# Kernel optimization log

Measured on AMD Instinct MI355X. Metric: run time of the kernel, lower is better.

Reference implementation:

```python
import jax, jax.numpy as jnp
import numpy as np

N = 100000   # active voxels
K = 27       # 3x3x3 kernel offsets
C = 64       # in_channels == out_channels (residual block)
EPS = 1e-5


def setup_inputs() -> dict:
    key = jax.random.key(0)
    ks = jax.random.split(key, 10)
    feats = jax.random.normal(ks[0], (N, C), dtype=jnp.float32)
    # kernel-map: for each voxel, index of the neighbor voxel for each of the 27 offsets
    nbr = jax.random.randint(ks[1], (N, K), 0, N)
    nbr = nbr.at[:, K // 2].set(jnp.arange(N))  # center offset is identity
    w_scale = 1.0 / np.sqrt(K * C)
    W1 = jax.random.normal(ks[2], (K, C, C), dtype=jnp.float32) * w_scale
    b1 = jax.random.normal(ks[3], (C,), dtype=jnp.float32) * 0.01
    g1 = jnp.ones((C,), jnp.float32)
    be1 = jnp.zeros((C,), jnp.float32)
    W2 = jax.random.normal(ks[4], (K, C, C), dtype=jnp.float32) * w_scale
    b2 = jax.random.normal(ks[5], (C,), dtype=jnp.float32) * 0.01
    g2 = jnp.ones((C,), jnp.float32)
    be2 = jnp.zeros((C,), jnp.float32)
    return {"feats": feats, "nbr": nbr, "W1": W1, "b1": b1, "g1": g1, "be1": be1,
            "W2": W2, "b2": b2, "g2": g2, "be2": be2}


def _sparse_conv(f, nbr, W, b):
    # gather neighbor features per kernel offset: [N, K, C]
    g = f[nbr]
    # per-offset matmul and reduce over offsets (gather-matmul-scatter form)
    return jnp.einsum('nkc,kcd->nd', g, W) + b


def _bn(x, gamma, beta):
    # BatchNorm over active voxels (training-mode batch stats, per channel)
    mu = x.mean(axis=0)
    var = x.var(axis=0)
    return (x - mu) * jax.lax.rsqrt(var + EPS) * gamma + beta


def reference(feats, nbr, W1, b1, g1, be1, W2, b2, g2, be2):
    h = jax.nn.relu(_bn(_sparse_conv(feats, nbr, W1, b1), g1, be1))
    h = _bn(_sparse_conv(h, nbr, W2, b2), g2, be2)
    return jax.nn.relu(h + feats)  # residual add + ReLU
```

## Files before the change

kernel.cpp:

```cpp
#include <hip/hip_runtime.h>

#define NCH 64
#define KOFF 27
#define EPSV 1e-5f

typedef __attribute__((ext_vector_type(8))) short  bf16x8;
typedef __attribute__((ext_vector_type(4))) float  f32x4;
typedef __attribute__((ext_vector_type(8))) unsigned short u16x8;

__device__ __forceinline__ unsigned short f2bf(float x) {
    unsigned int u = __float_as_uint(x);
    u += 0x7fffu + ((u >> 16) & 1u);
    return (unsigned short)(u >> 16);
}

__global__ __launch_bounds__(256)
void prep_kernel(const float* __restrict__ feats,
                 const float* __restrict__ W1, const float* __restrict__ W2,
                 unsigned short* __restrict__ fbf,
                 unsigned short* __restrict__ wt1, unsigned short* __restrict__ wt2,
                 float* __restrict__ stat, int total8)
{
    const int b = blockIdx.x;
    if (b == 0) {
        stat[threadIdx.x] = 0.f;
        return;
    }
    if (b <= 108) {
        const float* W = (b <= 54) ? W1 : W2;
        unsigned short* Wt = (b <= 54) ? wt1 : wt2;
        const int t = (b <= 54 ? b - 1 : b - 55) * 256 + threadIdx.x;
        const int l  = t & 63;
        const int ct = (t >> 6) & 3;
        const int s  = (t >> 8) & 1;
        const int k  = t >> 9;
        const int d     = ct * 16 + (l & 15);
        const int cbase = s * 32 + (l >> 4) * 8;
        u16x8 o;
#pragma unroll
        for (int j = 0; j < 8; ++j)
            o[j] = f2bf(W[(size_t)k * 4096 + (size_t)(cbase + j) * 64 + d]);
        reinterpret_cast<u16x8*>(Wt)[t] = o;
        return;
    }
    const int idx = (b - 109) * 256 + threadIdx.x;
    if (idx >= total8) return;
    const float4* xp = reinterpret_cast<const float4*>(feats) + (size_t)idx * 2;
    const float4 a = xp[0], c = xp[1];
    u16x8 o;
    o[0] = f2bf(a.x); o[1] = f2bf(a.y); o[2] = f2bf(a.z); o[3] = f2bf(a.w);
    o[4] = f2bf(c.x); o[5] = f2bf(c.y); o[6] = f2bf(c.z); o[7] = f2bf(c.w);
    reinterpret_cast<u16x8*>(fbf)[idx] = o;
}

__global__ __launch_bounds__(64, 3)
void conv_mfma_kernel(const unsigned short* __restrict__ fin,
                      const int* __restrict__ nbr,
                      const unsigned short* __restrict__ Wt,
                      const float* __restrict__ bias,
                      float* __restrict__ out, float* __restrict__ pstat, int N)
{
    __shared__ int s_idx[32 * KOFF];

    const int lane = threadIdx.x;
    const int n0   = blockIdx.x * 32;
    const int m    = lane & 15;
    const int quad = lane >> 4;

    {
        const int rem  = N - n0;
        const int maxi = (rem < 32 ? rem : 32) * KOFF;
        const int* nb  = nbr + (size_t)n0 * KOFF;
        for (int p = lane; p < 32 * KOFF; p += 64)
            s_idx[p] = ((p < maxi) ? nb[p] : 0) * (NCH * 2);
    }

    f32x4 acc[2][4];
#pragma unroll
    for (int mt = 0; mt < 2; ++mt)
#pragma unroll
        for (int ct = 0; ct < 4; ++ct) acc[mt][ct] = (f32x4){0.f, 0.f, 0.f, 0.f};

    bf16x8 A[2][2][2];
    bf16x8 B[2][2][4];
    const char* finB = (const char*)fin;

#define LOADK(kk, p)                                                         \
    {                                                                        \
        _Pragma("unroll")                                                    \
        for (int mt = 0; mt < 2; ++mt) {                                     \
            const int ofs = s_idx[(mt * 16 + m) * KOFF + (kk)];              \
            const char* fp = finB + ofs + quad * 16;                         \
            A[p][mt][0] = *reinterpret_cast<const bf16x8*>(fp);              \
            A[p][mt][1] = *reinterpret_cast<const bf16x8*>(fp + 64);         \
        }                                                                    \
        const unsigned short* wp = Wt + (size_t)(kk) * 4096 + lane * 8;      \
        _Pragma("unroll")                                                    \
        for (int s = 0; s < 2; ++s)                                          \
            _Pragma("unroll")                                                \
            for (int ct = 0; ct < 4; ++ct)                                   \
                B[p][s][ct] =                                                \
                    *reinterpret_cast<const bf16x8*>(wp + (s * 4 + ct) * 512);\
    }

#define DOMFMA(p)                                                            \
    {                                                                        \
        _Pragma("unroll")                                                    \
        for (int mt = 0; mt < 2; ++mt)                                       \
            _Pragma("unroll")                                                \
            for (int s = 0; s < 2; ++s)                                      \
                _Pragma("unroll")                                            \
                for (int ct = 0; ct < 4; ++ct)                               \
                    acc[mt][ct] = __builtin_amdgcn_mfma_f32_16x16x32_bf16(   \
                        A[p][mt][s], B[p][s][ct], acc[mt][ct], 0, 0, 0);     \
    }

    LOADK(0, 0);
#pragma unroll 1
    for (int k = 0; k + 2 < KOFF; k += 2) {
        LOADK(k + 1, 1);
        DOMFMA(0);
        LOADK(k + 2, 0);
        DOMFMA(1);
    }
    DOMFMA(0);

#pragma unroll
    for (int ct = 0; ct < 4; ++ct) {
        const int ch = ct * 16 + m;
        const float bv = bias[ch];
        float s = 0.f, q = 0.f;
#pragma unroll
        for (int mt = 0; mt < 2; ++mt) {
#pragma unroll
            for (int r = 0; r < 4; ++r) {
                const int vox = n0 + mt * 16 + quad * 4 + r;
                if (vox < N) {
                    const float v = acc[mt][ct][r] + bv;
                    out[(size_t)vox * NCH + ch] = v;
                    s += v;
                    q += v * v;
                }
            }
        }
        s += __shfl_xor(s, 16, 64);
        s += __shfl_xor(s, 32, 64);
        q += __shfl_xor(q, 16, 64);
        q += __shfl_xor(q, 32, 64);
        if (quad == 0) {
            float* pr = pstat + (size_t)blockIdx.x * 128;
            pr[ch]      = s;
            pr[64 + ch] = q;
        }
    }
#undef LOADK
#undef DOMFMA
}

__global__ __launch_bounds__(256)
void reduce_stats_kernel(const float* __restrict__ pstat, float* __restrict__ stat,
                         int rows)
{
    __shared__ float s_[256];
    const int ch = threadIdx.x & 127;
    const int h  = threadIdx.x >> 7;
    float acc = 0.f;
    for (int r = blockIdx.x * 2 + h; r < rows; r += gridDim.x * 2)
        acc += pstat[(size_t)r * 128 + ch];
    s_[threadIdx.x] = acc;
    __syncthreads();
    if (threadIdx.x < 128)
        atomicAdd(&stat[threadIdx.x], s_[threadIdx.x] + s_[threadIdx.x + 128]);
}

__global__ __launch_bounds__(256)
void bn_relu_bf16_kernel(const float* __restrict__ x, const float* __restrict__ sums,
                         const float* __restrict__ gmm, const float* __restrict__ bet,
                         float invN, unsigned short* __restrict__ y, int total8)
{
    const int idx = blockIdx.x * 256 + threadIdx.x;
    if (idx >= total8) return;
    const int c0 = (idx & 7) * 8;
    const float4* xp = reinterpret_cast<const float4*>(x) + (size_t)idx * 2;
    const float4 a = xp[0], b = xp[1];
    float v[8] = {a.x, a.y, a.z, a.w, b.x, b.y, b.z, b.w};
    u16x8 o;
#pragma unroll
    for (int i = 0; i < 8; ++i) {
        const int c = c0 + i;
        const float mu  = sums[c] * invN;
        const float var = sums[64 + c] * invN - mu * mu;
        const float rs  = rsqrtf(var + EPSV);
        const float sc  = gmm[c] * rs;
        const float sh  = bet[c] - mu * sc;
        o[i] = f2bf(fmaxf(fmaf(v[i], sc, sh), 0.f));
    }
    reinterpret_cast<u16x8*>(y)[idx] = o;
}

__global__ __launch_bounds__(256)
void bn_res_relu_kernel(float* __restrict__ x, const float* __restrict__ feats,
                        const float* __restrict__ sums, const float* __restrict__ gmm,
                        const float* __restrict__ bet, float invN, int total4)
{
    const int idx = blockIdx.x * blockDim.x + threadIdx.x;
    if (idx >= total4) return;
    float4 v = reinterpret_cast<float4*>(x)[idx];
    const float4 f = reinterpret_cast<const float4*>(feats)[idx];
    const int c0 = (idx & 15) * 4;
    float sc[4], sh[4];
#pragma unroll
    for (int i = 0; i < 4; ++i) {
        const int c = c0 + i;
        const float mu  = sums[c] * invN;
        const float var = sums[64 + c] * invN - mu * mu;
        const float rs  = rsqrtf(var + EPSV);
        sc[i] = gmm[c] * rs;
        sh[i] = bet[c] - mu * sc[i];
    }
    v.x = fmaxf(fmaf(v.x, sc[0], sh[0]) + f.x, 0.f);
    v.y = fmaxf(fmaf(v.y, sc[1], sh[1]) + f.y, 0.f);
    v.z = fmaxf(fmaf(v.z, sc[2], sh[2]) + f.z, 0.f);
    v.w = fmaxf(fmaf(v.w, sc[3], sh[3]) + f.w, 0.f);
    reinterpret_cast<float4*>(x)[idx] = v;
}

extern "C" void kernel_launch(void* const* d_in, const int* in_sizes, int n_in,
                              void* d_out, int out_size, void* d_ws, size_t ws_size,
                              hipStream_t stream)
{
    const float* feats = (const float*)d_in[0];
    const int*   nbr   = (const int*)d_in[1];
    const float* W1    = (const float*)d_in[2];
    const float* b1    = (const float*)d_in[3];
    const float* g1    = (const float*)d_in[4];
    const float* be1   = (const float*)d_in[5];
    const float* W2    = (const float*)d_in[6];
    const float* b2    = (const float*)d_in[7];
    const float* g2    = (const float*)d_in[8];
    const float* be2   = (const float*)d_in[9];
    float* out = (float*)d_out;

    const int N  = in_sizes[0] / NCH;
    const int NC = N * NCH;
    const float invN = 1.0f / (float)N;

    float*          h0   = (float*)d_ws;
    unsigned short* fbf  = (unsigned short*)(h0 + NC);
    unsigned short* hbf  = fbf + NC;
    unsigned short* wt1  = hbf + NC;
    unsigned short* wt2  = wt1 + KOFF * 4096;
    float*          stat = (float*)(wt2 + KOFF * 4096);

    const int total8   = NC / 8;
    const int castGrid = (total8 + 255) / 256;
    const int prepGrid = 1 + 108 + castGrid;
    const int convGrid = (N + 31) / 32;

    float* pstat1 = out;
    float* pstat2 = h0;

    prep_kernel<<<prepGrid, 256, 0, stream>>>(feats, W1, W2, fbf, wt1, wt2,
                                              stat, total8);
    conv_mfma_kernel<<<convGrid, 64, 0, stream>>>(fbf, nbr, wt1, b1, h0,
                                                  pstat1, N);
    reduce_stats_kernel<<<32, 256, 0, stream>>>(pstat1, stat, convGrid);
    bn_relu_bf16_kernel<<<castGrid, 256, 0, stream>>>(h0, stat, g1, be1, invN,
                                                      hbf, total8);
    conv_mfma_kernel<<<convGrid, 64, 0, stream>>>(hbf, nbr, wt2, b2, out,
                                                  pstat2, N);
    reduce_stats_kernel<<<32, 256, 0, stream>>>(pstat2, stat + 128, convGrid);
    bn_res_relu_kernel<<<(NC / 4 + 255) / 256, 256, 0, stream>>>(
        out, feats, stat + 128, g2, be2, invN, NC / 4);
}
```

Measured before the change: 296.0 us.

## Deepen gather prefetch pipeline with separate A and B ring buffers

Splits each kernel offset into two K-halves and software-pipelines the loop fully unrolled over 54 steps. Gathered neighbor loads (A) are prefetched 6 steps ahead in a 7-slot ring and weight loads (B) 2 steps ahead in a 3-slot ring. The aim is to hide the latency of the random gathers better than the previous double buffer. The deeper ring and full unroll raise register pressure and code size, which could lower occupancy.

Result: faster. 287.3 us (-3.0%).

```diff
diff --git a/kernel.cpp b/kernel.cpp
--- a/kernel.cpp
+++ b/kernel.cpp
@@ -81,49 +81,48 @@
 #pragma unroll
         for (int ct = 0; ct < 4; ++ct) acc[mt][ct] = (f32x4){0.f, 0.f, 0.f, 0.f};
 
-    bf16x8 A[2][2][2];
-    bf16x8 B[2][2][4];
+    bf16x8 A[7][2];
+    bf16x8 B[3][4];
     const char* finB = (const char*)fin;
 
-#define LOADK(kk, p)                                                         \
+#define LOADA(t, buf)                                                        \
     {                                                                        \
+        const int k_ = (t) >> 1, s_ = (t) & 1;                               \
         _Pragma("unroll")                                                    \
         for (int mt = 0; mt < 2; ++mt) {                                     \
-            const int ofs = s_idx[(mt * 16 + m) * KOFF + (kk)];              \
-            const char* fp = finB + ofs + quad * 16;                         \
-            A[p][mt][0] = *reinterpret_cast<const bf16x8*>(fp);              \
-            A[p][mt][1] = *reinterpret_cast<const bf16x8*>(fp + 64);         \
+            const int ofs = s_idx[(mt * 16 + m) * KOFF + k_];                \
+            A[buf][mt] = *reinterpret_cast<const bf16x8*>(                   \
+                finB + ofs + s_ * 64 + quad * 16);                           \
         }                                                                    \
-        const unsigned short* wp = Wt + (size_t)(kk) * 4096 + lane * 8;      \
+    }
+
+#define LOADB(t, buf)                                                        \
+    {                                                                        \
+        const unsigned short* wp = Wt + (size_t)(t) * 2048 + lane * 8;       \
         _Pragma("unroll")                                                    \
-        for (int s = 0; s < 2; ++s)                                          \
-            _Pragma("unroll")                                                \
-            for (int ct = 0; ct < 4; ++ct)                                   \
-                B[p][s][ct] =                                                \
-                    *reinterpret_cast<const bf16x8*>(wp + (s * 4 + ct) * 512);\
-    }
-
-#define DOMFMA(p)                                                            \
+        for (int ct = 0; ct < 4; ++ct)                                       \
+            B[buf][ct] = *reinterpret_cast<const bf16x8*>(wp + ct * 512);    \
+    }
+
+#define DOMFMA(t)                                                            \
     {                                                                        \
         _Pragma("unroll")                                                    \
         for (int mt = 0; mt < 2; ++mt)                                       \
             _Pragma("unroll")                                                \
-            for (int s = 0; s < 2; ++s)                                      \
-                _Pragma("unroll")                                            \
-                for (int ct = 0; ct < 4; ++ct)                               \
-                    acc[mt][ct] = __builtin_amdgcn_mfma_f32_16x16x32_bf16(   \
-                        A[p][mt][s], B[p][s][ct], acc[mt][ct], 0, 0, 0);     \
-    }
-
-    LOADK(0, 0);
-#pragma unroll 1
-    for (int k = 0; k + 2 < KOFF; k += 2) {
-        LOADK(k + 1, 1);
-        DOMFMA(0);
-        LOADK(k + 2, 0);
-        DOMFMA(1);
-    }
-    DOMFMA(0);
+            for (int ct = 0; ct < 4; ++ct)                                   \
+                acc[mt][ct] = __builtin_amdgcn_mfma_f32_16x16x32_bf16(       \
+                    A[(t) % 7][mt], B[(t) % 3][ct], acc[mt][ct], 0, 0, 0);   \
+    }
+
+    LOADA(0, 0); LOADA(1, 1); LOADA(2, 2);
+    LOADA(3, 3); LOADA(4, 4); LOADA(5, 5);
+    LOADB(0, 0); LOADB(1, 1);
+#pragma unroll
+    for (int t = 0; t < 2 * KOFF; ++t) {
+        if (t + 6 < 2 * KOFF) LOADA(t + 6, (t + 6) % 7);
+        if (t + 2 < 2 * KOFF) LOADB(t + 2, (t + 2) % 3);
+        DOMFMA(t);
+    }
 
 #pragma unroll
     for (int ct = 0; ct < 4; ++ct) {
@@ -153,7 +152,8 @@
             pr[64 + ch] = q;
         }
     }
-#undef LOADK
+#undef LOADA
+#undef LOADB
 #undef DOMFMA
 }
 
```

## Split kernel offsets across two waves per block and fuse BN stats via atomics

Applied to the files above, without the earlier changes.

The conv kernel now uses two wavefronts per 32-voxel tile, each covering half of the 27 kernel offsets (14 and 13). The partial accumulators are combined through shared memory before bias is added and the output is written. Per-block BN sums are added directly into the global stat buffer with atomics, so the separate reduce_stats kernels and their launches are gone. This doubles the waves available to hide gather latency, at the cost of an LDS round-trip, a block sync, and atomic contention on 128 addresses from about 3125 blocks.

Result: slower. 469.4 us (+58.6%).

```diff
diff --git a/kernel.cpp b/kernel.cpp
--- a/kernel.cpp
+++ b/kernel.cpp
@@ -53,16 +53,18 @@
     reinterpret_cast<u16x8*>(fbf)[idx] = o;
 }
 
-__global__ __launch_bounds__(64, 3)
+__global__ __launch_bounds__(128, 6)
 void conv_mfma_kernel(const unsigned short* __restrict__ fin,
                       const int* __restrict__ nbr,
                       const unsigned short* __restrict__ Wt,
                       const float* __restrict__ bias,
-                      float* __restrict__ out, float* __restrict__ pstat, int N)
-{
-    __shared__ int s_idx[32 * KOFF];
-
-    const int lane = threadIdx.x;
+                      float* __restrict__ out, float* __restrict__ stat, int N)
+{
+    __shared__ int   s_idx[32 * KOFF];
+    __shared__ float s_comb[32 * NCH];
+
+    const int lane = threadIdx.x & 63;
+    const int wv   = threadIdx.x >> 6;
     const int n0   = blockIdx.x * 32;
     const int m    = lane & 15;
     const int quad = lane >> 4;
@@ -71,8 +73,9 @@
         const int rem  = N - n0;
         const int maxi = (rem < 32 ? rem : 32) * KOFF;
         const int* nb  = nbr + (size_t)n0 * KOFF;
-        for (int p = lane; p < 32 * KOFF; p += 64)
+        for (int p = threadIdx.x; p < 32 * KOFF; p += 128)
             s_idx[p] = ((p < maxi) ? nb[p] : 0) * (NCH * 2);
+        __syncthreads();
     }
 
     f32x4 acc[2][4];
@@ -115,62 +118,68 @@
                         A[p][mt][s], B[p][s][ct], acc[mt][ct], 0, 0, 0);     \
     }
 
-    LOADK(0, 0);
+    const int kbeg = wv * 14;
+    const int kend = wv ? KOFF : 14;
+    LOADK(kbeg, 0);
+    int k = kbeg;
 #pragma unroll 1
-    for (int k = 0; k + 2 < KOFF; k += 2) {
+    for (; k + 2 < kend; k += 2) {
         LOADK(k + 1, 1);
         DOMFMA(0);
         LOADK(k + 2, 0);
         DOMFMA(1);
     }
-    DOMFMA(0);
-
-#pragma unroll
-    for (int ct = 0; ct < 4; ++ct) {
-        const int ch = ct * 16 + m;
-        const float bv = bias[ch];
-        float s = 0.f, q = 0.f;
-#pragma unroll
-        for (int mt = 0; mt < 2; ++mt) {
-#pragma unroll
-            for (int r = 0; r < 4; ++r) {
-                const int vox = n0 + mt * 16 + quad * 4 + r;
-                if (vox < N) {
-                    const float v = acc[mt][ct][r] + bv;
-                    out[(size_t)vox * NCH + ch] = v;
-                    s += v;
-                    q += v * v;
+    if (k + 1 < kend) {
+        LOADK(k + 1, 1);
+        DOMFMA(0);
+        DOMFMA(1);
+    } else {
+        DOMFMA(0);
+    }
+#undef LOADK
+#undef DOMFMA
+
+    if (wv == 1) {
+#pragma unroll
+        for (int mt = 0; mt < 2; ++mt)
+#pragma unroll
+            for (int ct = 0; ct < 4; ++ct)
+#pragma unroll
+                for (int r = 0; r < 4; ++r)
+                    s_comb[(mt * 16 + quad * 4 + r) * NCH + ct * 16 + m] =
+                        acc[mt][ct][r];
+    }
+    __syncthreads();
+    if (wv == 0) {
+#pragma unroll
+        for (int ct = 0; ct < 4; ++ct) {
+            const int ch = ct * 16 + m;
+            const float bv = bias[ch];
+            float s = 0.f, q = 0.f;
+#pragma unroll
+            for (int mt = 0; mt < 2; ++mt) {
+#pragma unroll
+                for (int r = 0; r < 4; ++r) {
+                    const int lv  = mt * 16 + quad * 4 + r;
+                    const int vox = n0 + lv;
+                    if (vox < N) {
+                        const float v = acc[mt][ct][r] + s_comb[lv * NCH + ch] + bv;
+                        out[(size_t)vox * NCH + ch] = v;
+                        s += v;
+                        q += v * v;
+                    }
                 }
             }
+            s += __shfl_xor(s, 16, 64);
+            s += __shfl_xor(s, 32, 64);
+            q += __shfl_xor(q, 16, 64);
+            q += __shfl_xor(q, 32, 64);
+            if (quad == 0) {
+                atomicAdd(&stat[ch],      s);
+                atomicAdd(&stat[64 + ch], q);
+            }
         }
-        s += __shfl_xor(s, 16, 64);
-        s += __shfl_xor(s, 32, 64);
-        q += __shfl_xor(q, 16, 64);
-        q += __shfl_xor(q, 32, 64);
-        if (quad == 0) {
-            float* pr = pstat + (size_t)blockIdx.x * 128;
-            pr[ch]      = s;
-            pr[64 + ch] = q;
-        }
-    }
-#undef LOADK
-#undef DOMFMA
-}
-
-__global__ __launch_bounds__(256)
-void reduce_stats_kernel(const float* __restrict__ pstat, float* __restrict__ stat,
-                         int rows)
-{
-    __shared__ float s_[256];
-    const int ch = threadIdx.x & 127;
-    const int h  = threadIdx.x >> 7;
-    float acc = 0.f;
-    for (int r = blockIdx.x * 2 + h; r < rows; r += gridDim.x * 2)
-        acc += pstat[(size_t)r * 128 + ch];
-    s_[threadIdx.x] = acc;
-    __syncthreads();
-    if (threadIdx.x < 128)
-        atomicAdd(&stat[threadIdx.x], s_[threadIdx.x] + s_[threadIdx.x + 128]);
+    }
 }
 
 __global__ __launch_bounds__(256)
@@ -257,19 +266,14 @@
     const int prepGrid = 1 + 108 + castGrid;
     const int convGrid = (N + 31) / 32;
 
-    float* pstat1 = out;
-    float* pstat2 = h0;
-
     prep_kernel<<<prepGrid, 256, 0, stream>>>(feats, W1, W2, fbf, wt1, wt2,
                                               stat, total8);
-    conv_mfma_kernel<<<convGrid, 64, 0, stream>>>(fbf, nbr, wt1, b1, h0,
-                                                  pstat1, N);
-    reduce_stats_kernel<<<32, 256, 0, stream>>>(pstat1, stat, convGrid);
+    conv_mfma_kernel<<<convGrid, 128, 0, stream>>>(fbf, nbr, wt1, b1, h0,
+                                                   stat, N);
     bn_relu_bf16_kernel<<<castGrid, 256, 0, stream>>>(h0, stat, g1, be1, invN,
                                                       hbf, total8);
-    conv_mfma_kernel<<<convGrid, 64, 0, stream>>>(hbf, nbr, wt2, b2, out,
-                                                  pstat2, N);
-    reduce_stats_kernel<<<32, 256, 0, stream>>>(pstat2, stat + 128, convGrid);
+    conv_mfma_kernel<<<convGrid, 128, 0, stream>>>(hbf, nbr, wt2, b2, out,
+                                                   stat + 128, N);
     bn_res_relu_kernel<<<(NC / 4 + 255) / 256, 256, 0, stream>>>(
         out, feats, stat + 128, g2, be2, invN, NC / 4);
 }
```

## Split kernel offsets across two waves per block and combine via LDS

Applied to the files above, without the earlier changes.

The sparse conv kernel now runs two wavefronts per 32-voxel block. Each wave handles half of the 27 kernel offsets, and the partial accumulators are combined through shared memory before the bias, store and stats epilogue. This doubles parallelism per voxel tile and roughly halves the serial offset loop length, aiming to hide the latency of gathered loads. Weight loads are no longer double-buffered, which lowers register pressure, and sched barriers are added. The cost is an extra LDS round-trip, two block barriers, and an idle second wave during the epilogue.

Result: no change. 292.0 us (-1.3%).

```diff
diff --git a/kernel.cpp b/kernel.cpp
--- a/kernel.cpp
+++ b/kernel.cpp
@@ -53,16 +53,18 @@
     reinterpret_cast<u16x8*>(fbf)[idx] = o;
 }
 
-__global__ __launch_bounds__(64, 3)
+__global__ __launch_bounds__(128, 4)
 void conv_mfma_kernel(const unsigned short* __restrict__ fin,
                       const int* __restrict__ nbr,
                       const unsigned short* __restrict__ Wt,
                       const float* __restrict__ bias,
                       float* __restrict__ out, float* __restrict__ pstat, int N)
 {
-    __shared__ int s_idx[32 * KOFF];
-
-    const int lane = threadIdx.x;
+    __shared__ int   s_idx[32 * KOFF];
+    __shared__ f32x4 s_comb4[8][64];
+
+    const int lane = threadIdx.x & 63;
+    const int wv   = threadIdx.x >> 6;
     const int n0   = blockIdx.x * 32;
     const int m    = lane & 15;
     const int quad = lane >> 4;
@@ -71,9 +73,10 @@
         const int rem  = N - n0;
         const int maxi = (rem < 32 ? rem : 32) * KOFF;
         const int* nb  = nbr + (size_t)n0 * KOFF;
-        for (int p = lane; p < 32 * KOFF; p += 64)
+        for (int p = threadIdx.x; p < 32 * KOFF; p += 128)
             s_idx[p] = ((p < maxi) ? nb[p] : 0) * (NCH * 2);
     }
+    __syncthreads();
 
     f32x4 acc[2][4];
 #pragma unroll
@@ -82,10 +85,10 @@
         for (int ct = 0; ct < 4; ++ct) acc[mt][ct] = (f32x4){0.f, 0.f, 0.f, 0.f};
 
     bf16x8 A[2][2][2];
-    bf16x8 B[2][2][4];
+    bf16x8 B[2][4];
     const char* finB = (const char*)fin;
 
-#define LOADK(kk, p)                                                         \
+#define LOADA(kk, p)                                                         \
     {                                                                        \
         _Pragma("unroll")                                                    \
         for (int mt = 0; mt < 2; ++mt) {                                     \
@@ -94,12 +97,16 @@
             A[p][mt][0] = *reinterpret_cast<const bf16x8*>(fp);              \
             A[p][mt][1] = *reinterpret_cast<const bf16x8*>(fp + 64);         \
         }                                                                    \
+    }
+
+#define LOADB(kk)                                                            \
+    {                                                                        \
         const unsigned short* wp = Wt + (size_t)(kk) * 4096 + lane * 8;      \
         _Pragma("unroll")                                                    \
         for (int s = 0; s < 2; ++s)                                          \
             _Pragma("unroll")                                                \
             for (int ct = 0; ct < 4; ++ct)                                   \
-                B[p][s][ct] =                                                \
+                B[s][ct] =                                                   \
                     *reinterpret_cast<const bf16x8*>(wp + (s * 4 + ct) * 512);\
     }
 
@@ -112,49 +119,78 @@
                 _Pragma("unroll")                                            \
                 for (int ct = 0; ct < 4; ++ct)                               \
                     acc[mt][ct] = __builtin_amdgcn_mfma_f32_16x16x32_bf16(   \
-                        A[p][mt][s], B[p][s][ct], acc[mt][ct], 0, 0, 0);     \
-    }
-
-    LOADK(0, 0);
+                        A[p][mt][s], B[s][ct], acc[mt][ct], 0, 0, 0);        \
+    }
+
+    const int kbeg = wv ? 14 : 0;
+    const int kend = wv ? KOFF : 14;
+    LOADA(kbeg, 0);
+    int k = kbeg;
 #pragma unroll 1
-    for (int k = 0; k + 2 < KOFF; k += 2) {
-        LOADK(k + 1, 1);
+    for (; k + 2 < kend; k += 2) {
+        LOADB(k);
+        LOADA(k + 1, 1);
+        __builtin_amdgcn_sched_barrier(0);
         DOMFMA(0);
-        LOADK(k + 2, 0);
+        LOADB(k + 1);
+        LOADA(k + 2, 0);
+        __builtin_amdgcn_sched_barrier(0);
         DOMFMA(1);
     }
-    DOMFMA(0);
-
-#pragma unroll
-    for (int ct = 0; ct < 4; ++ct) {
-        const int ch = ct * 16 + m;
-        const float bv = bias[ch];
-        float s = 0.f, q = 0.f;
-#pragma unroll
-        for (int mt = 0; mt < 2; ++mt) {
-#pragma unroll
-            for (int r = 0; r < 4; ++r) {
-                const int vox = n0 + mt * 16 + quad * 4 + r;
-                if (vox < N) {
-                    const float v = acc[mt][ct][r] + bv;
-                    out[(size_t)vox * NCH + ch] = v;
-                    s += v;
-                    q += v * v;
+    if (k + 1 < kend) {
+        LOADB(k);
+        LOADA(k + 1, 1);
+        __builtin_amdgcn_sched_barrier(0);
+        DOMFMA(0);
+        LOADB(k + 1);
+        DOMFMA(1);
+    } else {
+        LOADB(k);
+        DOMFMA(0);
+    }
+#undef LOADA
+#undef LOADB
+#undef DOMFMA
+
+    if (wv == 1) {
+#pragma unroll
+        for (int mt = 0; mt < 2; ++mt)
+#pragma unroll
+            for (int ct = 0; ct < 4; ++ct)
+                s_comb4[mt * 4 + ct][lane] = acc[mt][ct];
+    }
+    __syncthreads();
+    if (wv == 0) {
+#pragma unroll
+        for (int ct = 0; ct < 4; ++ct) {
+            const int ch = ct * 16 + m;
+            const float bv = bias[ch];
+            float s = 0.f, q = 0.f;
+#pragma unroll
+            for (int mt = 0; mt < 2; ++mt) {
+                const f32x4 part = s_comb4[mt * 4 + ct][lane];
+#pragma unroll
+                for (int r = 0; r < 4; ++r) {
+                    const int vox = n0 + mt * 16 + quad * 4 + r;
+                    if (vox < N) {
+                        const float v = acc[mt][ct][r] + part[r] + bv;
+                        out[(size_t)vox * NCH + ch] = v;
+                        s += v;
+                        q += v * v;
+                    }
                 }
             }
+            s += __shfl_xor(s, 16, 64);
+            s += __shfl_xor(s, 32, 64);
+            q += __shfl_xor(q, 16, 64);
+            q += __shfl_xor(q, 32, 64);
+            if (quad == 0) {
+                float* pr = pstat + (size_t)blockIdx.x * 128;
+                pr[ch]      = s;
+                pr[64 + ch] = q;
+            }
         }
-        s += __shfl_xor(s, 16, 64);
-        s += __shfl_xor(s, 32, 64);
-        q += __shfl_xor(q, 16, 64);
-        q += __shfl_xor(q, 32, 64);
-        if (quad == 0) {
-            float* pr = pstat + (size_t)blockIdx.x * 128;
-            pr[ch]      = s;
-            pr[64 + ch] = q;
-        }
-    }
-#undef LOADK
-#undef DOMFMA
+    }
 }
 
 __global__ __launch_bounds__(256)
@@ -262,13 +298,13 @@
 
     prep_kernel<<<prepGrid, 256, 0, stream>>>(feats, W1, W2, fbf, wt1, wt2,
                                               stat, total8);
-    conv_mfma_kernel<<<convGrid, 64, 0, stream>>>(fbf, nbr, wt1, b1, h0,
-                                                  pstat1, N);
+    conv_mfma_kernel<<<convGrid, 128, 0, stream>>>(fbf, nbr, wt1, b1, h0,
+                                                   pstat1, N);
     reduce_stats_kernel<<<32, 256, 0, stream>>>(pstat1, stat, convGrid);
     bn_relu_bf16_kernel<<<castGrid, 256, 0, stream>>>(h0, stat, g1, be1, invN,
                                                       hbf, total8);
-    conv_mfma_kernel<<<convGrid, 64, 0, stream>>>(hbf, nbr, wt2, b2, out,
-                                                  pstat2, N);
+    conv_mfma_kernel<<<convGrid, 128, 0, stream>>>(hbf, nbr, wt2, b2, out,
+                                                   pstat2, N);
     reduce_stats_kernel<<<32, 256, 0, stream>>>(pstat2, stat + 128, convGrid);
     bn_res_relu_kernel<<<(NC / 4 + 255) / 256, 256, 0, stream>>>(
         out, feats, stat + 128, g2, be2, invN, NC / 4);
```
